# Kernel tuning notes

Measured on AMD Instinct MI355X. Metric: run time of the kernel, lower is better.

Reference implementation:

```python
import jax, jax.numpy as jnp
import numpy as np

NEG_SLOPE = 0.2  # PyG GATConv default negative_slope
EPS = 1e-16     # PyG softmax denominator epsilon


def gat_layer(x, src, dst, W, att_src, att_dst, bias, N):
    """PyG-style GATConv: gather -> leaky-relu score -> segment softmax -> scatter-add.
    x: [N, F_in], W: [F_in, H*C], att_src/att_dst: [H, C], bias: [H*C].
    src/dst: [E] edge endpoints (messages flow src -> dst), self-loops included.
    """
    H, C = att_src.shape
    h = (x @ W).reshape(N, H, C)                       # [N, H, C]
    a_s = jnp.sum(h * att_src, axis=-1)                # [N, H]
    a_d = jnp.sum(h * att_dst, axis=-1)                # [N, H]
    e = a_s[src] + a_d[dst]                            # [E, H]
    e = jnp.where(e > 0, e, NEG_SLOPE * e)             # leaky relu
    m = jax.ops.segment_max(e, dst, num_segments=N)    # [N, H] (self-loops ensure every node hit)
    p = jnp.exp(e - m[dst])                            # [E, H]
    s = jax.ops.segment_sum(p, dst, num_segments=N)    # [N, H]
    alpha = p / (s[dst] + EPS)                         # [E, H]
    out = jax.ops.segment_sum(alpha[:, :, None] * h[src], dst, num_segments=N)  # [N, H, C]
    return out.reshape(N, H * C) + bias


def setup_inputs() -> dict:
    key = jax.random.key(0)
    ks = jax.random.split(key, 12)
    N, E = 100000, 1600000
    x = jax.random.normal(ks[0], (N, 1), dtype=jnp.float32)
    edge_index = jax.random.randint(ks[1], (2, E), 0, N, dtype=jnp.int32)
    sc = 0.1
    # conv1: in=1, heads=4, out=8
    W1 = jax.random.normal(ks[2], (1, 32), dtype=jnp.float32) * sc
    att_src1 = jax.random.normal(ks[3], (4, 8), dtype=jnp.float32) * sc
    att_dst1 = jax.random.normal(ks[4], (4, 8), dtype=jnp.float32) * sc
    bias1 = jnp.zeros((32,), dtype=jnp.float32)
    # conv2: in=32, heads=8, out=8
    W2 = jax.random.normal(ks[5], (32, 64), dtype=jnp.float32) * sc
    att_src2 = jax.random.normal(ks[6], (8, 8), dtype=jnp.float32) * sc
    att_dst2 = jax.random.normal(ks[7], (8, 8), dtype=jnp.float32) * sc
    bias2 = jnp.zeros((64,), dtype=jnp.float32)
    # fc2: 64 -> 1
    fc_w = jax.random.normal(ks[8], (64, 1), dtype=jnp.float32) * sc
    fc_b = jnp.zeros((1,), dtype=jnp.float32)
    return {"x": x, "edge_index": edge_index,
            "W1": W1, "att_src1": att_src1, "att_dst1": att_dst1, "bias1": bias1,
            "W2": W2, "att_src2": att_src2, "att_dst2": att_dst2, "bias2": bias2,
            "fc_w": fc_w, "fc_b": fc_b}


def reference(x, edge_index, W1, att_src1, att_dst1, bias1,
              W2, att_src2, att_dst2, bias2, fc_w, fc_b):
    N = x.shape[0]
    loop = jnp.arange(N, dtype=edge_index.dtype)       # add_self_loops=True (PyG default)
    src = jnp.concatenate([edge_index[0], loop])
    dst = jnp.concatenate([edge_index[1], loop])
    h = jax.nn.elu(gat_layer(x, src, dst, W1, att_src1, att_dst1, bias1, N))
    h = jax.nn.elu(gat_layer(h, src, dst, W2, att_src2, att_dst2, bias2, N))
    return h @ fc_w + fc_b                             # [N, 1]
```

## Files before the change

### kernel.cpp

```cpp
#include <hip/hip_runtime.h>
#include <hip/hip_fp16.h>
#include <cmath>

#define TPB 256
#define STPB 512
#define NSLOPE 0.2f
#define SEPS 1e-16f

#define BSH 7
#define BNODES 128
#define NBMAX 1024
#define NCHUNK2 512
#define SCTPB 1024
#define CAP 32
#define STAGE 4608
#define MAXDEG 96

__device__ __forceinline__ float lrelu(float v) { return v > 0.f ? v : NSLOPE * v; }
__device__ __forceinline__ float elu1(float v)  { return v > 0.f ? v : expm1f(v); }
__device__ __forceinline__ float elu1f(float v) { return v > 0.f ? v : __expf(v) - 1.f; }

__global__ void k_bscatter(const int* __restrict__ srcI, const int* __restrict__ dstI,
                           int E, int NB, int chunk,
                           int* __restrict__ pk, unsigned char* __restrict__ cnt8) {
    __shared__ int cntL[NBMAX];
    int t = threadIdx.x;
    int c = blockIdx.x;
    int beg = c * chunk;
    int end = min(beg + chunk, E);
    for (int i = t; i < NBMAX; i += SCTPB) cntL[i] = 0;
    __syncthreads();
    for (int e = beg + t; e < end; e += SCTPB) {
        int s = srcI[e], d = dstI[e];
        int b = d >> BSH;
        int r = atomicAdd(&cntL[b], 1);
        if (r < CAP)
            pk[((size_t)b * NCHUNK2 + c) * CAP + r] = (s << BSH) | (d & (BNODES - 1));
    }
    __syncthreads();
    for (int i = t; i < NB; i += SCTPB)
        cnt8[(size_t)i * NCHUNK2 + c] = (unsigned char)min(cntL[i], CAP);
}

__global__ void k_sl1h2(const int* __restrict__ pk, const unsigned char* __restrict__ cnt8,
                        unsigned cap,
                        const float* __restrict__ x,
                        const float* __restrict__ as1, const float* __restrict__ ad1,
                        const float* __restrict__ W1, const float* __restrict__ b1,
                        const float* __restrict__ W2, const float* __restrict__ attS,
                        const float* __restrict__ attD, int N,
                        unsigned* __restrict__ offsets, int* __restrict__ sortedSrc,
                        __half* __restrict__ h2h, float* __restrict__ aS, float* __restrict__ aD) {
    __shared__ __align__(16) char upool[BNODES * 36 * 4];
    int* praw = (int*)upool;
    float (*lds1)[36] = (float (*)[36])upool;
    __shared__ int sorted[STAGE];
    __shared__ int cnt[BNODES];
    __shared__ int offl[BNODES];
    __shared__ float SDs[8];
    __shared__ int wt8[8], wo8[8];
    __shared__ int mTot, w0tot;
    int b = blockIdx.x, t = threadIdx.x;
    int lane = t & 63, wv = t >> 6;
    int base = b << BSH;
    unsigned rbeg = (unsigned)b * cap;
    if (t < BNODES) cnt[t] = (base + t < N) ? 1 : 0;
    if (t < 8) {
        int h = t & 3;
        const float* att = (t >= 4) ? ad1 : as1;
        float acc = 0.f;
        #pragma unroll
        for (int cc = 0; cc < 8; ++cc) acc += W1[h*8+cc] * att[h*8+cc];
        SDs[t] = acc;
    }
    int myc = (int)cnt8[(size_t)b * NCHUNK2 + t];
    int inc2 = myc;
    #pragma unroll
    for (int off = 1; off < 64; off <<= 1) {
        int u = __shfl_up(inc2, off);
        if (lane >= off) inc2 += u;
    }
    if (lane == 63) wt8[wv] = inc2;
    __syncthreads();
    if (t < 8) {
        int xv = wt8[t];
        int sc_ = xv;
        #pragma unroll
        for (int off = 1; off < 8; off <<= 1) {
            int u = __shfl_up(sc_, off);
            if (t >= off) sc_ += u;
        }
        wo8[t] = sc_ - xv;
        if (t == 7) mTot = sc_;
    }
    __syncthreads();
    int segOff = inc2 + wo8[wv] - myc;
    if (segOff + myc > STAGE) myc = max(0, STAGE - segOff);
    {
        const int* seg = pk + ((size_t)b * NCHUNK2 + t) * CAP;
        for (int j = 0; j < myc; ++j) {
            int p = seg[j];
            praw[segOff + j] = p;
            atomicAdd(&cnt[p & (BNODES - 1)], 1);
        }
        if (t < BNODES && base + t < N && mTot + t < STAGE)
            praw[mTot + t] = ((base + t) << BSH) | t;
    }
    __syncthreads();
    int m = min(mTot + min(BNODES, N - base), STAGE);
    int v = (t < BNODES) ? cnt[t] : 0;
    int inc = v;
    #pragma unroll
    for (int off = 1; off < 64; off <<= 1) {
        int u = __shfl_up(inc, off);
        if (lane >= off) inc += u;
    }
    if (t == 63) w0tot = inc;
    __syncthreads();
    if (t >= 64 && t < BNODES) inc += w0tot;
    if (t < BNODES) {
        int ex = inc - v;
        int d = base + t;
        if (d < N) offsets[d] = ((rbeg + (unsigned)ex) << 10) | (unsigned)v;
        cnt[t] = 0;
        offl[t] = ex;
    }
    __syncthreads();
    for (int i = t; i < m; i += STPB) {
        int p = praw[i];
        int dl = p & (BNODES - 1);
        int r = atomicAdd(&cnt[dl], 1);
        sorted[offl[dl] + r] = p >> BSH;
    }
    __syncthreads();
    for (int i = t; i < m; i += STPB) sortedSrc[rbeg + i] = sorted[i];
    __syncthreads();
    int n = t >> 2, q = t & 3;
    int d2 = base + n;
    bool active = (d2 < N);
    float s0 = 0.f, s1 = 0.f, s2 = 0.f, s3 = 0.f;
    float g0 = 0.f, g1 = 0.f, g2 = 0.f, g3 = 0.f;
    if (active) {
        int deg = cnt[n];
        int lbeg = offl[n];
        float xd = x[d2];
        float S0 = SDs[0], S1 = SDs[1], S2 = SDs[2], S3 = SDs[3];
        float D0 = xd*SDs[4], D1 = xd*SDs[5], D2 = xd*SDs[6], D3 = xd*SDs[7];
        int dq = (deg + 3) >> 2;
        int i = lbeg + q * dq;
        int rem = min(dq, deg - q * dq);
        for (; rem >= 2; rem -= 2, i += 2) {
            int a0 = sorted[i];
            int a1 = sorted[i + 1];
            float x0 = x[a0], x1 = x[a1];
            float p;
            p = __expf(lrelu(x0*S0 + D0)); s0 += p; g0 += p * x0;
            p = __expf(lrelu(x0*S1 + D1)); s1 += p; g1 += p * x0;
            p = __expf(lrelu(x0*S2 + D2)); s2 += p; g2 += p * x0;
            p = __expf(lrelu(x0*S3 + D3)); s3 += p; g3 += p * x0;
            p = __expf(lrelu(x1*S0 + D0)); s0 += p; g0 += p * x1;
            p = __expf(lrelu(x1*S1 + D1)); s1 += p; g1 += p * x1;
            p = __expf(lrelu(x1*S2 + D2)); s2 += p; g2 += p * x1;
            p = __expf(lrelu(x1*S3 + D3)); s3 += p; g3 += p * x1;
        }
        if (rem > 0) {
            int a0 = sorted[i];
            float xs = x[a0];
            float p;
            p = __expf(lrelu(xs*S0 + D0)); s0 += p; g0 += p * xs;
            p = __expf(lrelu(xs*S1 + D1)); s1 += p; g1 += p * xs;
            p = __expf(lrelu(xs*S2 + D2)); s2 += p; g2 += p * xs;
            p = __expf(lrelu(xs*S3 + D3)); s3 += p; g3 += p * xs;
        }
    }
    s0 += __shfl_xor(s0, 1); s1 += __shfl_xor(s1, 1);
    s2 += __shfl_xor(s2, 1); s3 += __shfl_xor(s3, 1);
    g0 += __shfl_xor(g0, 1); g1 += __shfl_xor(g1, 1);
    g2 += __shfl_xor(g2, 1); g3 += __shfl_xor(g3, 1);
    s0 += __shfl_xor(s0, 2); s1 += __shfl_xor(s1, 2);
    s2 += __shfl_xor(s2, 2); s3 += __shfl_xor(s3, 2);
    g0 += __shfl_xor(g0, 2); g1 += __shfl_xor(g1, 2);
    g2 += __shfl_xor(g2, 2); g3 += __shfl_xor(g3, 2);
    if (active) {
        float gq = (q == 0) ? g0 / (s0 + SEPS) :
                   (q == 1) ? g1 / (s1 + SEPS) :
                   (q == 2) ? g2 / (s2 + SEPS) :
                              g3 / (s3 + SEPS);
        #pragma unroll
        for (int cc = 0; cc < 8; ++cc)
            lds1[n][q*8+cc] = elu1(gq * W1[q*8+cc] + b1[q*8+cc]);
    }
    __syncthreads();
    int sub = t >> 6;
    float w2r[32];
    #pragma unroll
    for (int k = 0; k < 32; ++k) w2r[k] = W2[k*64 + lane];
    float attSl = attS[lane], attDl = attD[lane];
    int nCnt = min(BNODES, N - base);
    for (int nn = sub; nn < nCnt; nn += 8) {
        const float4* row4 = (const float4*)lds1[nn];
        float acc = 0.f;
        #pragma unroll
        for (int k4 = 0; k4 < 8; ++k4) {
            float4 rv = row4[k4];
            acc += rv.x*w2r[4*k4] + rv.y*w2r[4*k4+1] + rv.z*w2r[4*k4+2] + rv.w*w2r[4*k4+3];
        }
        int node = base + nn;
        h2h[(size_t)node*64 + lane] = __float2half(acc);
        float ps = acc * attSl;
        float pd = acc * attDl;
        #pragma unroll
        for (int mm = 1; mm < 8; mm <<= 1) {
            ps += __shfl_xor(ps, mm);
            pd += __shfl_xor(pd, mm);
        }
        int hh = lane >> 3, cc = lane & 7;
        if (cc == 0) aS[(size_t)node*8 + hh] = ps;
        if (cc == 1) aD[(size_t)node*8 + hh] = pd;
    }
}

__global__ void k_agg(const unsigned* __restrict__ offsets, const int* __restrict__ ss,
                      const float* __restrict__ aS, const float* __restrict__ aD,
                      const __half* __restrict__ h2h, const float* __restrict__ b2,
                      const float* __restrict__ fcw, const float* __restrict__ fcb,
                      float* __restrict__ out, int N) {
    __shared__ int sl[4][MAXDEG];
    int lane = threadIdx.x & 63;
    int w = threadIdx.x >> 6;
    int d = blockIdx.x * 4 + w;
    if (d >= N) return;
    unsigned u = offsets[d];
    unsigned beg = u >> 10;
    int deg = (int)(u & 1023u);
    int lH   = lane & 31;
    int half = lane >> 5;
    int hh   = lH >> 2;
    const __half2* __restrict__ hp = (const __half2*)h2h;
    float sum = 0.f, ax = 0.f, ay = 0.f;
    if (deg <= MAXDEG) {
        int degPad = (deg + 7) & ~7;
        for (int j = lane; j < degPad; j += 64) sl[w][j] = ss[beg + (unsigned)min(j, deg - 1)];
        float adv = aD[(unsigned)d * 8u + (unsigned)hh];
        for (int e = 0; e < degPad; e += 8) {
            int bi = e + half;
            int s0 = sl[w][bi],     s1 = sl[w][bi + 2];
            int s2 = sl[w][bi + 4], s3 = sl[w][bi + 6];
            float a0 = aS[(unsigned)s0 * 8u + (unsigned)hh];
            float a1 = aS[(unsigned)s1 * 8u + (unsigned)hh];
            float a2 = aS[(unsigned)s2 * 8u + (unsigned)hh];
            float a3 = aS[(unsigned)s3 * 8u + (unsigned)hh];
            float2 g0 = __half22float2(hp[(unsigned)s0 * 32u + (unsigned)lH]);
            float2 g1 = __half22float2(hp[(unsigned)s1 * 32u + (unsigned)lH]);
            float2 g2 = __half22float2(hp[(unsigned)s2 * 32u + (unsigned)lH]);
            float2 g3 = __half22float2(hp[(unsigned)s3 * 32u + (unsigned)lH]);
            float p0 = __expf(lrelu(a0 + adv));
            float p1 = __expf(lrelu(a1 + adv));
            float p2 = __expf(lrelu(a2 + adv));
            float p3 = __expf(lrelu(a3 + adv));
            if (e + 8 > deg) {
                if (bi     >= deg) p0 = 0.f;
                if (bi + 2 >= deg) p1 = 0.f;
                if (bi + 4 >= deg) p2 = 0.f;
                if (bi + 6 >= deg) p3 = 0.f;
            }
            ax += p0*g0.x + p1*g1.x + p2*g2.x + p3*g3.x;
            ay += p0*g0.y + p1*g1.y + p2*g2.y + p3*g3.y;
            sum += (p0 + p1) + (p2 + p3);
        }
    } else {
        float adh = aD[(size_t)d*8 + hh];
        for (int e = half; e < deg; e += 2) {
            int s = ss[beg + e];
            float p = __expf(lrelu(aS[(size_t)s*8 + hh] + adh));
            float2 g = __half22float2(*(const __half2*)(h2h + (size_t)s*64 + 2*lH));
            ax += p*g.x; ay += p*g.y; sum += p;
        }
    }
    ax  += __shfl_xor(ax, 32);
    ay  += __shfl_xor(ay, 32);
    sum += __shfl_xor(sum, 32);
    float inv = 1.f / (sum + SEPS);
    float tt = elu1f(ax*inv + b2[2*lH]) * fcw[2*lH]
             + elu1f(ay*inv + b2[2*lH+1]) * fcw[2*lH+1];
    #pragma unroll
    for (int m = 16; m; m >>= 1) tt += __shfl_xor(tt, m);
    if (lane == 0) out[d] = tt + fcb[0];
}

extern "C" void kernel_launch(void* const* d_in, const int* in_sizes, int n_in,
                              void* d_out, int out_size, void* d_ws, size_t ws_size,
                              hipStream_t stream) {
    const float* x    = (const float*)d_in[0];
    const int*   ei   = (const int*)  d_in[1];
    const float* W1   = (const float*)d_in[2];
    const float* as1  = (const float*)d_in[3];
    const float* ad1  = (const float*)d_in[4];
    const float* b1   = (const float*)d_in[5];
    const float* W2   = (const float*)d_in[6];
    const float* attS2= (const float*)d_in[7];
    const float* attD2= (const float*)d_in[8];
    const float* b2   = (const float*)d_in[9];
    const float* fcw  = (const float*)d_in[10];
    const float* fcb  = (const float*)d_in[11];
    float* out = (float*)d_out;

    int N = in_sizes[0];
    int E = in_sizes[1] / 2;
    int ET = E + N;
    int NB = (N + BNODES - 1) / BNODES;
    unsigned cap = (unsigned)((ET + NB - 1) / NB + 512);
    cap = (cap + 3u) & ~3u;

    const int* srcI = ei;
    const int* dstI = ei + E;

    float* ws = (float*)d_ws;
    size_t off = 0;
    int*      pk        = (int*)(ws + off); off += (size_t)NB * NCHUNK2 * CAP;
    unsigned char* cnt8 = (unsigned char*)(ws + off); off += ((size_t)NB * NCHUNK2 + 3) / 4;
    unsigned* offsets   = (unsigned*)(ws + off); off += (size_t)N + 16;
    int*      sortedSrc = (int*)(ws + off); off += (size_t)NB * cap;
    float*    aS2       = ws + off; off += (size_t)N * 8;
    float*    aD2       = ws + off; off += (size_t)N * 8;
    off = (off + 31) & ~(size_t)31;
    __half*   h2h       = (__half*)(ws + off); off += (size_t)N * 32;

    int chunk = (E + NCHUNK2 - 1) / NCHUNK2;
    k_bscatter<<<NCHUNK2, SCTPB, 0, stream>>>(srcI, dstI, E, NB, chunk, pk, cnt8);
    k_sl1h2   <<<NB, STPB, 0, stream>>>(pk, cnt8, cap, x, as1, ad1, W1, b1,
                                        W2, attS2, attD2,
                                        N, offsets, sortedSrc, h2h, aS2, aD2);
    k_agg     <<<(N + 3) / 4, TPB, 0, stream>>>(offsets, sortedSrc, aS2, aD2, h2h,
                                                b2, fcw, fcb, out, N);
}
```

Baseline: 206.8 us.

## Halve bucket chunks and load packed edge slab with coalesced int4 reads

Halves the number of chunks per node bucket, so each chunk holds twice as many edges and there are half as many per-chunk counters. The bucket-sort kernel now reads the whole packed slab with coalesced int4 loads across all threads, instead of each thread walking its own segment serially. Per-chunk counts and bases are staged in shared memory so threads can locate their elements. The aim is to remove uncoalesced, divergent global reads. The trade-offs are fewer scatter blocks (less parallelism) and a higher chance of per-chunk CAP overflow, since edges per chunk double.

```diff
diff --git a/kernel.cpp b/kernel.cpp
--- a/kernel.cpp
+++ b/kernel.cpp
@@ -10,7 +10,7 @@
 #define BSH 7
 #define BNODES 128
 #define NBMAX 1024
-#define NCHUNK2 512
+#define NCHUNK2 256
 #define SCTPB 1024
 #define CAP 32
 #define STAGE 4608
@@ -57,8 +57,10 @@
     __shared__ int sorted[STAGE];
     __shared__ int cnt[BNODES];
     __shared__ int offl[BNODES];
+    __shared__ int scnt[NCHUNK2];
+    __shared__ int sbase[NCHUNK2];
     __shared__ float SDs[8];
-    __shared__ int wt8[8], wo8[8];
+    __shared__ int wt4[4], wo4[4];
     __shared__ int mTot, w0tot;
     int b = blockIdx.x, t = threadIdx.x;
     int lane = t & 63, wv = t >> 6;
@@ -73,35 +75,48 @@
         for (int cc = 0; cc < 8; ++cc) acc += W1[h*8+cc] * att[h*8+cc];
         SDs[t] = acc;
     }
-    int myc = (int)cnt8[(size_t)b * NCHUNK2 + t];
+    int myc = (t < NCHUNK2) ? (int)cnt8[(size_t)b * NCHUNK2 + t] : 0;
     int inc2 = myc;
     #pragma unroll
     for (int off = 1; off < 64; off <<= 1) {
         int u = __shfl_up(inc2, off);
         if (lane >= off) inc2 += u;
     }
-    if (lane == 63) wt8[wv] = inc2;
-    __syncthreads();
-    if (t < 8) {
-        int xv = wt8[t];
+    if (t < NCHUNK2 && lane == 63) wt4[wv] = inc2;
+    __syncthreads();
+    if (t < 4) {
+        int xv = wt4[t];
         int sc_ = xv;
         #pragma unroll
-        for (int off = 1; off < 8; off <<= 1) {
+        for (int off = 1; off < 4; off <<= 1) {
             int u = __shfl_up(sc_, off);
             if (t >= off) sc_ += u;
         }
-        wo8[t] = sc_ - xv;
-        if (t == 7) mTot = sc_;
-    }
-    __syncthreads();
-    int segOff = inc2 + wo8[wv] - myc;
-    if (segOff + myc > STAGE) myc = max(0, STAGE - segOff);
+        wo4[t] = sc_ - xv;
+        if (t == 3) mTot = sc_;
+    }
+    __syncthreads();
+    if (t < NCHUNK2) {
+        scnt[t] = myc;
+        sbase[t] = inc2 + wo4[wv] - myc;
+    }
+    __syncthreads();
     {
-        const int* seg = pk + ((size_t)b * NCHUNK2 + t) * CAP;
-        for (int j = 0; j < myc; ++j) {
-            int p = seg[j];
-            praw[segOff + j] = p;
-            atomicAdd(&cnt[p & (BNODES - 1)], 1);
+        const int4* slab = (const int4*)(pk + (size_t)b * NCHUNK2 * CAP);
+        for (int i4 = t; i4 < NCHUNK2 * CAP / 4; i4 += STPB) {
+            int4 v = slab[i4];
+            int c = i4 >> 3;
+            int j0 = (i4 & 7) << 2;
+            int cv = scnt[c];
+            if (j0 < cv) {
+                int sb = sbase[c];
+                int nv = min(4, cv - j0);
+                int vv0 = v.x, vv1 = v.y, vv2 = v.z, vv3 = v.w;
+                if (0 < nv && sb + j0 + 0 < STAGE) { praw[sb + j0 + 0] = vv0; atomicAdd(&cnt[vv0 & (BNODES - 1)], 1); }
+                if (1 < nv && sb + j0 + 1 < STAGE) { praw[sb + j0 + 1] = vv1; atomicAdd(&cnt[vv1 & (BNODES - 1)], 1); }
+                if (2 < nv && sb + j0 + 2 < STAGE) { praw[sb + j0 + 2] = vv2; atomicAdd(&cnt[vv2 & (BNODES - 1)], 1); }
+                if (3 < nv && sb + j0 + 3 < STAGE) { praw[sb + j0 + 3] = vv3; atomicAdd(&cnt[vv3 & (BNODES - 1)], 1); }
+            }
         }
         if (t < BNODES && base + t < N && mTot + t < STAGE)
             praw[mTot + t] = ((base + t) << BSH) | t;
```

New measurement: 188.0 us (median of 2 runs). 1.1x faster.
